# Optimization experiments

Measured on AMD Instinct MI355X. Metric: run time of the kernel, lower is better.

Reference implementation:

```python
import jax, jax.numpy as jnp
import numpy as np

C = 128
NUM_HEADS = 8
KEY_DIM = C // NUM_HEADS  # 16
BN_EPS = 1e-5


def setup_inputs() -> dict:
    key = jax.random.key(0)
    ks = jax.random.split(key, 6)
    B, H, W = 8, 32, 32
    stddev = KEY_DIM ** (-0.5)
    return {
        "x": jax.random.normal(ks[0], (B, C, H, W), dtype=jnp.float32),
        "gamma": jnp.ones((C,), dtype=jnp.float32),
        "beta": jnp.zeros((C,), dtype=jnp.float32),
        "wq": jax.random.normal(ks[1], (C, C), dtype=jnp.float32) * 0.05,
        "wk": jax.random.normal(ks[2], (C, C), dtype=jnp.float32) * 0.05,
        "wv": jax.random.normal(ks[3], (C, C), dtype=jnp.float32) * 0.05,
        "pos_emb_h": jax.random.uniform(ks[4], (2 * H - 1,), dtype=jnp.float32) * stddev,
        "pos_emb_w": jax.random.uniform(ks[5], (2 * W - 1,), dtype=jnp.float32) * stddev,
    }


def _rel_bias(pos_emb, L):
    # torch: pos_emb.unfold(0, L, 1).flip(-1) -> emb[i, k] = pos_emb[i + (L-1) - k]
    idx = jnp.arange(L)[:, None] + (L - 1) - jnp.arange(L)[None, :]
    return pos_emb[idx]  # [L, L]


def reference(x, gamma, beta, wq, wk, wv, pos_emb_h, pos_emb_w):
    B, _, H, W = x.shape
    N = H * W
    qk_scale = 1.0 / np.sqrt(np.float32(KEY_DIM))

    # BatchNorm2d (training-mode batch stats, biased variance) + exact GELU
    mean = jnp.mean(x, axis=(0, 2, 3), keepdims=True)
    var = jnp.var(x, axis=(0, 2, 3), keepdims=True)
    out = (x - mean) * jax.lax.rsqrt(var + BN_EPS)
    out = out * gamma[None, :, None, None] + beta[None, :, None, None]
    out = jax.nn.gelu(out, approximate=False)

    # 1x1 convs == per-pixel linear maps, then split heads and flatten spatial
    def proj(w):
        y = jnp.einsum('oc,bchw->bohw', w, out)
        return y.reshape(B, NUM_HEADS, KEY_DIM, N)  # [B, h, d, N]

    q = proj(wq) * qk_scale
    k = proj(wk)
    v = proj(wv)

    scores = jnp.einsum('bhdq,bhdk->bhqk', q, k)  # [B, h, N, N]

    h_emb = _rel_bias(pos_emb_h, H)  # [H, H]
    w_emb = _rel_bias(pos_emb_w, W)  # [W, W]
    emb = (h_emb[:, None, :, None] + w_emb[None, :, None, :]).reshape(N, N)
    scores = scores + emb[None, None, :, :]

    attn = jax.nn.softmax(scores, axis=-1)
    o = jnp.einsum('bhqk,bhdk->bhdq', attn, v)  # [B, h, d, N]
    o = o.reshape(B, C, H, W)
    return x + o
```

## Files before the change

kernel.cpp:

```cpp
#include <hip/hip_runtime.h>
#include <hip/hip_bf16.h>
#include <math.h>

typedef short bf4 __attribute__((ext_vector_type(4)));
typedef float f32x4 __attribute__((ext_vector_type(4)));

constexpr int CC  = 128;
constexpr int NH  = 8;
constexpr int KD  = 16;
constexpr int BB  = 8;
constexpr int NN  = 1024;
constexpr int BHW = BB * NN;
constexpr float LOG2E = 1.44269504088896340736f;
constexpr float MBOUND = 32.0f;

static __device__ __forceinline__ short f2bf(float x) {
    __hip_bfloat16 b = __float2bfloat16(x);
    short s;
    __builtin_memcpy(&s, &b, 2);
    return s;
}
static __device__ __forceinline__ unsigned fbits(float x) {
    unsigned u;
    __builtin_memcpy(&u, &x, 4);
    return u;
}
static __device__ __forceinline__ float fexp2(float x) {
#if __has_builtin(__builtin_amdgcn_exp2f)
    return __builtin_amdgcn_exp2f(x);
#else
    return exp2f(x);
#endif
}

static __device__ __forceinline__ f32x4 mfma16(bf4 a, bf4 b, f32x4 c) {
#if __has_builtin(__builtin_amdgcn_mfma_f32_16x16x16bf16_1k)
    return __builtin_amdgcn_mfma_f32_16x16x16bf16_1k(a, b, c, 0, 0, 0);
#else
    f32x4 d;
    asm volatile("v_mfma_f32_16x16x16_bf16 %0, %1, %2, %3"
                 : "=&v"(d) : "v"(a), "v"(b), "v"(c));
    return d;
#endif
}

__global__ __launch_bounds__(256) void k_prep(const float* __restrict__ x,
                                              const float* __restrict__ wq,
                                              const float* __restrict__ wk,
                                              const float* __restrict__ wv,
                                              float* __restrict__ ps,
                                              short* __restrict__ wf) {
    int t = threadIdx.x;
    int blk = blockIdx.x;
    if (blk < 1024) {
        int c = blk >> 3, b = blk & 7;
        float4 v = ((const float4*)(x + ((size_t)b * CC + c) * NN))[t];
        float s1 = v.x + v.y + v.z + v.w;
        float s2 = v.x * v.x + v.y * v.y + v.z * v.z + v.w * v.w;
        #pragma unroll
        for (int off = 32; off >= 1; off >>= 1) {
            s1 += __shfl_xor(s1, off);
            s2 += __shfl_xor(s2, off);
        }
        __shared__ float r1[4], r2[4];
        int wid = t >> 6, lane = t & 63;
        if (lane == 0) { r1[wid] = s1; r2[wid] = s2; }
        __syncthreads();
        if (t == 0) {
            ps[(c * 8 + b) * 2 + 0] = r1[0] + r1[1] + r1[2] + r1[3];
            ps[(c * 8 + b) * 2 + 1] = r2[0] + r2[1] + r2[2] + r2[3];
        }
    } else {
        int s = (blk - 1024) * 256 + t;
        int ln = s & 63, ct = (s >> 6) & 7, mt = (s >> 9) & 7, p = s >> 12;
        int hl = ln >> 4, li = ln & 15;
        const float* w = (p == 0) ? wq : (p == 1) ? wk : wv;
        float4 v = *(const float4*)(w + (size_t)(mt * 16 + li) * CC + ct * 16 + 4 * hl);
        float sc = (p == 0) ? 0.25f * LOG2E : 1.0f;
        bf4 r;
        r[0] = f2bf(v.x * sc); r[1] = f2bf(v.y * sc);
        r[2] = f2bf(v.z * sc); r[3] = f2bf(v.w * sc);
        *(bf4*)&wf[(size_t)s * 4] = r;
    }
}

__global__ __launch_bounds__(512) void k_proj(const float* __restrict__ x,
                                              const float* __restrict__ ps,
                                              const float* __restrict__ gamma,
                                              const float* __restrict__ beta,
                                              const short* __restrict__ wf,
                                              short* __restrict__ qf,
                                              short* __restrict__ kf,
                                              short* __restrict__ vf) {
    __shared__ float xS[128][20];
    __shared__ float ssS[256];
    __shared__ short afS[8][256];
    int it = blockIdx.x, b = blockIdx.y;
    int t = threadIdx.x;
    if (t < 128) {
        int c = t;
        const float4* pp = (const float4*)(ps + c * 16);
        float4 a0 = pp[0], a1 = pp[1], a2 = pp[2], a3 = pp[3];
        float s1 = a0.x + a0.z + a1.x + a1.z + a2.x + a2.z + a3.x + a3.z;
        float s2 = a0.y + a0.w + a1.y + a1.w + a2.y + a2.w + a3.y + a3.w;
        float mean = s1 / (float)BHW;
        float var  = s2 / (float)BHW - mean * mean;
        float rstd = rsqrtf(var + 1e-5f);
        float sc = rstd * gamma[c];
        ssS[c]       = sc;
        ssS[128 + c] = beta[c] - mean * sc;
    }
    const float* xb = x + (size_t)b * CC * NN + it * 16;
    {
        int r = t >> 2, cf = t & 3;
        float4 v = *(const float4*)(xb + (size_t)r * NN + cf * 4);
        *(float4*)&xS[r][cf * 4] = v;
    }
    __syncthreads();
    {
        int ct = t >> 6, ln = t & 63;
        int hl_ = ln >> 4, li_ = ln & 15;
        int c0 = ct * 16 + 4 * hl_;
        bf4 r;
        #pragma unroll
        for (int jj = 0; jj < 4; ++jj) {
            int c = c0 + jj;
            float v = xS[c][li_] * ssS[c] + ssS[128 + c];
            v = 0.5f * v * (1.0f + erff(v * 0.70710678f));
            r[jj] = f2bf(v);
        }
        *(bf4*)&afS[ct][ln * 4] = r;
    }
    __syncthreads();

    int wid = t >> 6, lane = t & 63;
    int hl = lane >> 4, li = lane & 15;
    f32x4 acc[3];
    #pragma unroll
    for (int e = 0; e < 3; ++e) acc[e] = (f32x4)0.f;
    #pragma unroll
    for (int ct = 0; ct < 8; ++ct) {
        bf4 af = *(const bf4*)&afS[ct][lane * 4];
        #pragma unroll
        for (int e = 0; e < 3; ++e) {
            int mtp = wid + 8 * e;
            bf4 wfr = *(const bf4*)(wf + ((size_t)(mtp * 8 + ct) * 64 + lane) * 4);
            acc[e] = mfma16(wfr, af, acc[e]);
        }
    }
    int bq = b * 8;
    #pragma unroll
    for (int e = 0; e < 2; ++e) {
        short* dst = (e == 0) ? qf : kf;
        bf4 r;
        #pragma unroll
        for (int jr = 0; jr < 4; ++jr) r[jr] = f2bf(acc[e][jr]);
        *(bf4*)&dst[(((size_t)(bq + wid) * 64 + it) * 64 + lane) * 4] = r;
    }
    {
        float* vScrW = &xS[0][0] + wid * 272;
        #pragma unroll
        for (int r = 0; r < 4; ++r)
            vScrW[(4 * hl + r) * 17 + li] = acc[2][r];
        bf4 r;
        #pragma unroll
        for (int jj = 0; jj < 4; ++jj)
            r[jj] = f2bf(vScrW[li * 17 + 4 * hl + jj]);
        *(bf4*)&vf[(((size_t)(bq + wid) * 64 + it) * 64 + lane) * 4] = r;
    }
}

__global__ __launch_bounds__(512) void k_attn(const short* __restrict__ qf,
                                              const short* __restrict__ kf,
                                              const short* __restrict__ vf,
                                              const float* __restrict__ x,
                                              const float* __restrict__ peh,
                                              const float* __restrict__ pew,
                                              float* __restrict__ out) {
    __shared__ short ldsK[16384];
    __shared__ short ldsV[16384];
    __shared__ float phS[64], pwS[64];
    int t = threadIdx.x;
    int bh = blockIdx.x;
    const short* qfh = qf + (size_t)bh * 16384;
    const short* kfh = kf + (size_t)bh * 16384;
    const short* vfh = vf + (size_t)bh * 16384;

    #pragma unroll
    for (int k = 0; k < 4; ++k)
        ((int4*)ldsK)[t + 512 * k] = ((const int4*)kfh)[t + 512 * k];
    #pragma unroll
    for (int k = 0; k < 4; ++k)
        ((int4*)ldsV)[t + 512 * k] = ((const int4*)vfh)[t + 512 * k];
    if (t < 64) {
        phS[t] = (t < 63) ? peh[t] * LOG2E : -1e30f;
        pwS[t] = (t < 63) ? pew[t] * LOG2E : -1e30f;
    }
    __syncthreads();

    int wid = t >> 6, lane = t & 63;
    int li = lane & 15, hl = lane >> 4;
    int it = blockIdx.y * 8 + wid;

    bf4 qfr = *(const bf4*)(qfh + ((size_t)it * 64 + lane) * 4);

    int wi = ((it & 1) << 4) | li;
    float pwm[2][4];
    #pragma unroll
    for (int jp = 0; jp < 2; ++jp)
        #pragma unroll
        for (int r = 0; r < 4; ++r)
            pwm[jp][r] = pwS[wi + 31 - ((jp << 4) + 4 * hl + r)] - MBOUND;

    int hq = it >> 1;
    const float* phBase = &phS[hq];
    const short* kBase = &ldsK[lane * 4];
    const short* vBase = &ldsV[lane * 4];

    f32x4 oaccA = (f32x4)0.f, oaccB = (f32x4)0.f;
    f32x4 lacc0 = (f32x4)0.f, lacc1 = (f32x4)0.f;
    short oneb = (short)0x3F80;
    bf4 ones = {oneb, oneb, oneb, oneb};

    auto qk = [&](int ch, f32x4* s) {
        float ph0 = phBase[31 - 2 * ch];
        float ph1 = phBase[30 - 2 * ch];
        #pragma unroll
        for (int jt = 0; jt < 4; ++jt) {
            bf4 kb = *(const bf4*)(kBase + (ch * 4 + jt) * 256);
            float ph = (jt < 2) ? ph0 : ph1;
            f32x4 c;
            #pragma unroll
            for (int r = 0; r < 4; ++r) c[r] = pwm[jt & 1][r] + ph;
            s[jt] = mfma16(kb, qfr, c);
        }
    };

    f32x4 s_cur[4];
    qk(0, s_cur);
    #pragma unroll
    for (int ch = 0; ch < 16; ++ch) {
        f32x4 s_nxt[4];
        if (ch < 15) qk(ch + 1, s_nxt);
        bf4 vb[4];
        #pragma unroll
        for (int jt = 0; jt < 4; ++jt)
            vb[jt] = *(const bf4*)(vBase + (ch * 4 + jt) * 256);
        #pragma unroll
        for (int jt = 0; jt < 4; ++jt)
            #pragma unroll
            for (int r = 0; r < 4; ++r)
                s_cur[jt][r] = fexp2(s_cur[jt][r]);
        bf4 pf[4];
        #pragma unroll
        for (int jt = 0; jt < 4; ++jt) {
            unsigned lo = __builtin_amdgcn_perm(fbits(s_cur[jt][1]), fbits(s_cur[jt][0]), 0x07060302u);
            unsigned hi = __builtin_amdgcn_perm(fbits(s_cur[jt][3]), fbits(s_cur[jt][2]), 0x07060302u);
            unsigned pk[2] = {lo, hi};
            __builtin_memcpy(&pf[jt], pk, 8);
        }
        oaccA = mfma16(vb[0], pf[0], oaccA);
        oaccB = mfma16(vb[2], pf[2], oaccB);
        lacc0 = mfma16(ones,  pf[0], lacc0);
        lacc1 = mfma16(ones,  pf[2], lacc1);
        oaccA = mfma16(vb[1], pf[1], oaccA);
        oaccB = mfma16(vb[3], pf[3], oaccB);
        lacc0 = mfma16(ones,  pf[1], lacc0);
        lacc1 = mfma16(ones,  pf[3], lacc1);
        #pragma unroll
        for (int jt = 0; jt < 4; ++jt) s_cur[jt] = s_nxt[jt];
    }

    float rl = 1.0f / (lacc0[0] + lacc1[0]);

    int b = bh >> 3, h = bh & 7;
    size_t base = (size_t)b * (CC * NN) + (size_t)h * KD * NN;
    int i = it * 16 + li;
    #pragma unroll
    for (int r = 0; r < 4; ++r) {
        int d = 4 * hl + r;
        size_t g = base + (size_t)d * NN + i;
        out[g] = x[g] + (oaccA[r] + oaccB[r]) * rl;
    }
}

extern "C" void kernel_launch(void* const* d_in, const int* in_sizes, int n_in,
                              void* d_out, int out_size, void* d_ws, size_t ws_size,
                              hipStream_t stream) {
    const float* x     = (const float*)d_in[0];
    const float* gamma = (const float*)d_in[1];
    const float* beta  = (const float*)d_in[2];
    const float* wq    = (const float*)d_in[3];
    const float* wk    = (const float*)d_in[4];
    const float* wv    = (const float*)d_in[5];
    const float* peh   = (const float*)d_in[6];
    const float* pew   = (const float*)d_in[7];
    float* out = (float*)d_out;
    float* ws  = (float*)d_ws;

    float* ps = ws;
    short* wf = (short*)(ws + 2048);
    short* qf = wf + 49152;
    short* kf = qf + (1 << 20);
    short* vf = kf + (1 << 20);

    k_prep<<<1072, 256, 0, stream>>>(x, wq, wk, wv, ps, wf);
    k_proj<<<dim3(64, 8), 512, 0, stream>>>(x, ps, gamma, beta, wf, qf, kf, vf);
    k_attn<<<dim3(64, 8), 512, 0, stream>>>(qf, kf, vf, x, peh, pew, out);
}
```

Measured before the change: 32.72 us.

## Stage K/V into LDS progressively and overlap staging with attention compute

The attention kernel now loads all K/V tiles into registers up front and writes them to LDS in four phases. Only the first quarter is made visible before compute begins, and each later quarter is stored while the current chunks are processed, with a barrier between phases. This hides the global-to-LDS staging latency behind the MFMA work. It also adds s_setprio around the PV MFMAs and a launch_bounds occupancy hint, at the cost of more registers held across the loop and extra barriers.

```diff
diff --git a/kernel.cpp b/kernel.cpp
--- a/kernel.cpp
+++ b/kernel.cpp
@@ -170,13 +170,13 @@
     }
 }
 
-__global__ __launch_bounds__(512) void k_attn(const short* __restrict__ qf,
-                                              const short* __restrict__ kf,
-                                              const short* __restrict__ vf,
-                                              const float* __restrict__ x,
-                                              const float* __restrict__ peh,
-                                              const float* __restrict__ pew,
-                                              float* __restrict__ out) {
+__global__ __launch_bounds__(512, 4) void k_attn(const short* __restrict__ qf,
+                                                 const short* __restrict__ kf,
+                                                 const short* __restrict__ vf,
+                                                 const float* __restrict__ x,
+                                                 const float* __restrict__ peh,
+                                                 const float* __restrict__ pew,
+                                                 float* __restrict__ out) {
     __shared__ short ldsK[16384];
     __shared__ short ldsV[16384];
     __shared__ float phS[64], pwS[64];
@@ -186,23 +186,25 @@
     const short* kfh = kf + (size_t)bh * 16384;
     const short* vfh = vf + (size_t)bh * 16384;
 
-    #pragma unroll
-    for (int k = 0; k < 4; ++k)
-        ((int4*)ldsK)[t + 512 * k] = ((const int4*)kfh)[t + 512 * k];
-    #pragma unroll
-    for (int k = 0; k < 4; ++k)
-        ((int4*)ldsV)[t + 512 * k] = ((const int4*)vfh)[t + 512 * k];
+    int4 kreg[4], vreg[4];
+    #pragma unroll
+    for (int k = 0; k < 4; ++k) kreg[k] = ((const int4*)kfh)[t + 512 * k];
+    #pragma unroll
+    for (int k = 0; k < 4; ++k) vreg[k] = ((const int4*)vfh)[t + 512 * k];
     if (t < 64) {
         phS[t] = (t < 63) ? peh[t] * LOG2E : -1e30f;
         pwS[t] = (t < 63) ? pew[t] * LOG2E : -1e30f;
     }
-    __syncthreads();
 
     int wid = t >> 6, lane = t & 63;
     int li = lane & 15, hl = lane >> 4;
     int it = blockIdx.y * 8 + wid;
-
     bf4 qfr = *(const bf4*)(qfh + ((size_t)it * 64 + lane) * 4);
+
+    ((int4*)ldsK)[t] = kreg[0];
+    ((int4*)ldsV)[t] = vreg[0];
+    asm volatile("s_waitcnt lgkmcnt(0)" ::: "memory");
+    __builtin_amdgcn_s_barrier();
 
     int wi = ((it & 1) << 4) | li;
     float pwm[2][4];
@@ -235,13 +237,7 @@
             s[jt] = mfma16(kb, qfr, c);
         }
     };
-
-    f32x4 s_cur[4];
-    qk(0, s_cur);
-    #pragma unroll
-    for (int ch = 0; ch < 16; ++ch) {
-        f32x4 s_nxt[4];
-        if (ch < 15) qk(ch + 1, s_nxt);
+    auto body = [&](f32x4* s_cur, int ch) {
         bf4 vb[4];
         #pragma unroll
         for (int jt = 0; jt < 4; ++jt)
@@ -259,6 +255,7 @@
             unsigned pk[2] = {lo, hi};
             __builtin_memcpy(&pf[jt], pk, 8);
         }
+        __builtin_amdgcn_s_setprio(1);
         oaccA = mfma16(vb[0], pf[0], oaccA);
         oaccB = mfma16(vb[2], pf[2], oaccB);
         lacc0 = mfma16(ones,  pf[0], lacc0);
@@ -267,8 +264,33 @@
         oaccB = mfma16(vb[3], pf[3], oaccB);
         lacc0 = mfma16(ones,  pf[1], lacc0);
         lacc1 = mfma16(ones,  pf[3], lacc1);
-        #pragma unroll
-        for (int jt = 0; jt < 4; ++jt) s_cur[jt] = s_nxt[jt];
+        __builtin_amdgcn_s_setprio(0);
+    };
+
+    f32x4 s_cur[4];
+    qk(0, s_cur);
+    #pragma unroll
+    for (int p = 0; p < 4; ++p) {
+        if (p < 3) {
+            ((int4*)ldsK)[t + 512 * (p + 1)] = kreg[p + 1];
+            ((int4*)ldsV)[t + 512 * (p + 1)] = vreg[p + 1];
+        }
+        #pragma unroll
+        for (int c = 0; c < 4; ++c) {
+            int ch = 4 * p + c;
+            f32x4 s_nxt[4];
+            if (c < 3) qk(ch + 1, s_nxt);
+            body(s_cur, ch);
+            if (c < 3) {
+                #pragma unroll
+                for (int jt = 0; jt < 4; ++jt) s_cur[jt] = s_nxt[jt];
+            }
+        }
+        if (p < 3) {
+            asm volatile("s_waitcnt lgkmcnt(0)" ::: "memory");
+            __builtin_amdgcn_s_barrier();
+            qk(4 * (p + 1), s_cur);
+        }
     }
 
     float rl = 1.0f / (lacc0[0] + lacc1[0]);
```

Result: no change. 32.78 us (+0.2%).

## Process two query tiles per wave in attention, reuse K/V fragments

Applied to the files above, without the earlier changes.

Each wave in the attention kernel now handles two 16-query tiles, so each K and V LDS fragment load feeds two MFMAs and the grid halves in y. The software-pipelined QK prefetch is removed in favour of interleaving the two independent tiles, and s_setprio is raised around the PV MFMA block. The projection kernel writes Q/K/V with nontemporal stores, and launch bounds now request 2 blocks per CU. Fewer workgroups and higher register pressure could reduce parallelism across the GPU.

```diff
diff --git a/kernel.cpp b/kernel.cpp
--- a/kernel.cpp
+++ b/kernel.cpp
@@ -155,7 +155,8 @@
         bf4 r;
         #pragma unroll
         for (int jr = 0; jr < 4; ++jr) r[jr] = f2bf(acc[e][jr]);
-        *(bf4*)&dst[(((size_t)(bq + wid) * 64 + it) * 64 + lane) * 4] = r;
+        __builtin_nontemporal_store(r,
+            (bf4*)&dst[(((size_t)(bq + wid) * 64 + it) * 64 + lane) * 4]);
     }
     {
         float* vScrW = &xS[0][0] + wid * 272;
@@ -166,17 +167,18 @@
         #pragma unroll
         for (int jj = 0; jj < 4; ++jj)
             r[jj] = f2bf(vScrW[li * 17 + 4 * hl + jj]);
-        *(bf4*)&vf[(((size_t)(bq + wid) * 64 + it) * 64 + lane) * 4] = r;
-    }
-}
-
-__global__ __launch_bounds__(512) void k_attn(const short* __restrict__ qf,
-                                              const short* __restrict__ kf,
-                                              const short* __restrict__ vf,
-                                              const float* __restrict__ x,
-                                              const float* __restrict__ peh,
-                                              const float* __restrict__ pew,
-                                              float* __restrict__ out) {
+        __builtin_nontemporal_store(r,
+            (bf4*)&vf[(((size_t)(bq + wid) * 64 + it) * 64 + lane) * 4]);
+    }
+}
+
+__global__ __launch_bounds__(512, 2) void k_attn(const short* __restrict__ qf,
+                                                 const short* __restrict__ kf,
+                                                 const short* __restrict__ vf,
+                                                 const float* __restrict__ x,
+                                                 const float* __restrict__ peh,
+                                                 const float* __restrict__ pew,
+                                                 float* __restrict__ out) {
     __shared__ short ldsK[16384];
     __shared__ short ldsV[16384];
     __shared__ float phS[64], pwS[64];
@@ -200,87 +202,104 @@
 
     int wid = t >> 6, lane = t & 63;
     int li = lane & 15, hl = lane >> 4;
-    int it = blockIdx.y * 8 + wid;
-
-    bf4 qfr = *(const bf4*)(qfh + ((size_t)it * 64 + lane) * 4);
-
-    int wi = ((it & 1) << 4) | li;
-    float pwm[2][4];
+    int it0 = (blockIdx.y * 8 + wid) * 2;
+
+    bf4 qfrA = *(const bf4*)(qfh + ((size_t)it0 * 64 + lane) * 4);
+    bf4 qfrB = *(const bf4*)(qfh + ((size_t)(it0 + 1) * 64 + lane) * 4);
+
+    float pwmA[2][4], pwmB[2][4];
     #pragma unroll
     for (int jp = 0; jp < 2; ++jp)
         #pragma unroll
-        for (int r = 0; r < 4; ++r)
-            pwm[jp][r] = pwS[wi + 31 - ((jp << 4) + 4 * hl + r)] - MBOUND;
-
-    int hq = it >> 1;
+        for (int r = 0; r < 4; ++r) {
+            int wj = (jp << 4) + 4 * hl + r;
+            pwmA[jp][r] = pwS[li + 31 - wj] - MBOUND;
+            pwmB[jp][r] = pwS[16 + li + 31 - wj] - MBOUND;
+        }
+
+    int hq = it0 >> 1;
     const float* phBase = &phS[hq];
     const short* kBase = &ldsK[lane * 4];
     const short* vBase = &ldsV[lane * 4];
 
-    f32x4 oaccA = (f32x4)0.f, oaccB = (f32x4)0.f;
-    f32x4 lacc0 = (f32x4)0.f, lacc1 = (f32x4)0.f;
+    f32x4 oA0 = (f32x4)0.f, oA1 = (f32x4)0.f, lA0 = (f32x4)0.f, lA1 = (f32x4)0.f;
+    f32x4 oB0 = (f32x4)0.f, oB1 = (f32x4)0.f, lB0 = (f32x4)0.f, lB1 = (f32x4)0.f;
     short oneb = (short)0x3F80;
     bf4 ones = {oneb, oneb, oneb, oneb};
 
-    auto qk = [&](int ch, f32x4* s) {
+    #pragma unroll
+    for (int ch = 0; ch < 16; ++ch) {
         float ph0 = phBase[31 - 2 * ch];
         float ph1 = phBase[30 - 2 * ch];
+        bf4 kb[4], vb[4];
         #pragma unroll
         for (int jt = 0; jt < 4; ++jt) {
-            bf4 kb = *(const bf4*)(kBase + (ch * 4 + jt) * 256);
+            kb[jt] = *(const bf4*)(kBase + (ch * 4 + jt) * 256);
+            vb[jt] = *(const bf4*)(vBase + (ch * 4 + jt) * 256);
+        }
+        f32x4 sA[4], sB[4];
+        #pragma unroll
+        for (int jt = 0; jt < 4; ++jt) {
             float ph = (jt < 2) ? ph0 : ph1;
-            f32x4 c;
+            f32x4 cA, cB;
             #pragma unroll
-            for (int r = 0; r < 4; ++r) c[r] = pwm[jt & 1][r] + ph;
-            s[jt] = mfma16(kb, qfr, c);
-        }
-    };
-
-    f32x4 s_cur[4];
-    qk(0, s_cur);
-    #pragma unroll
-    for (int ch = 0; ch < 16; ++ch) {
-        f32x4 s_nxt[4];
-        if (ch < 15) qk(ch + 1, s_nxt);
-        bf4 vb[4];
-        #pragma unroll
-        for (int jt = 0; jt < 4; ++jt)
-            vb[jt] = *(const bf4*)(vBase + (ch * 4 + jt) * 256);
+            for (int r = 0; r < 4; ++r) {
+                cA[r] = pwmA[jt & 1][r] + ph;
+                cB[r] = pwmB[jt & 1][r] + ph;
+            }
+            sA[jt] = mfma16(kb[jt], qfrA, cA);
+            sB[jt] = mfma16(kb[jt], qfrB, cB);
+        }
         #pragma unroll
         for (int jt = 0; jt < 4; ++jt)
             #pragma unroll
-            for (int r = 0; r < 4; ++r)
-                s_cur[jt][r] = fexp2(s_cur[jt][r]);
-        bf4 pf[4];
+            for (int r = 0; r < 4; ++r) {
+                sA[jt][r] = fexp2(sA[jt][r]);
+                sB[jt][r] = fexp2(sB[jt][r]);
+            }
+        bf4 pfA[4], pfB[4];
         #pragma unroll
         for (int jt = 0; jt < 4; ++jt) {
-            unsigned lo = __builtin_amdgcn_perm(fbits(s_cur[jt][1]), fbits(s_cur[jt][0]), 0x07060302u);
-            unsigned hi = __builtin_amdgcn_perm(fbits(s_cur[jt][3]), fbits(s_cur[jt][2]), 0x07060302u);
-            unsigned pk[2] = {lo, hi};
-            __builtin_memcpy(&pf[jt], pk, 8);
-        }
-        oaccA = mfma16(vb[0], pf[0], oaccA);
-        oaccB = mfma16(vb[2], pf[2], oaccB);
-        lacc0 = mfma16(ones,  pf[0], lacc0);
-        lacc1 = mfma16(ones,  pf[2], lacc1);
-        oaccA = mfma16(vb[1], pf[1], oaccA);
-        oaccB = mfma16(vb[3], pf[3], oaccB);
-        lacc0 = mfma16(ones,  pf[1], lacc0);
-        lacc1 = mfma16(ones,  pf[3], lacc1);
-        #pragma unroll
-        for (int jt = 0; jt < 4; ++jt) s_cur[jt] = s_nxt[jt];
-    }
-
-    float rl = 1.0f / (lacc0[0] + lacc1[0]);
+            unsigned loA = __builtin_amdgcn_perm(fbits(sA[jt][1]), fbits(sA[jt][0]), 0x07060302u);
+            unsigned hiA = __builtin_amdgcn_perm(fbits(sA[jt][3]), fbits(sA[jt][2]), 0x07060302u);
+            unsigned pkA[2] = {loA, hiA};
+            __builtin_memcpy(&pfA[jt], pkA, 8);
+            unsigned loB = __builtin_amdgcn_perm(fbits(sB[jt][1]), fbits(sB[jt][0]), 0x07060302u);
+            unsigned hiB = __builtin_amdgcn_perm(fbits(sB[jt][3]), fbits(sB[jt][2]), 0x07060302u);
+            unsigned pkB[2] = {loB, hiB};
+            __builtin_memcpy(&pfB[jt], pkB, 8);
+        }
+        __builtin_amdgcn_s_setprio(1);
+        oA0 = mfma16(vb[0], pfA[0], oA0);
+        oB0 = mfma16(vb[0], pfB[0], oB0);
+        oA1 = mfma16(vb[2], pfA[2], oA1);
+        oB1 = mfma16(vb[2], pfB[2], oB1);
+        lA0 = mfma16(ones,  pfA[0], lA0);
+        lB0 = mfma16(ones,  pfB[0], lB0);
+        lA1 = mfma16(ones,  pfA[2], lA1);
+        lB1 = mfma16(ones,  pfB[2], lB1);
+        oA0 = mfma16(vb[1], pfA[1], oA0);
+        oB0 = mfma16(vb[1], pfB[1], oB0);
+        oA1 = mfma16(vb[3], pfA[3], oA1);
+        oB1 = mfma16(vb[3], pfB[3], oB1);
+        lA0 = mfma16(ones,  pfA[1], lA0);
+        lB0 = mfma16(ones,  pfB[1], lB0);
+        lA1 = mfma16(ones,  pfA[3], lA1);
+        lB1 = mfma16(ones,  pfB[3], lB1);
+        __builtin_amdgcn_s_setprio(0);
+    }
+
+    float rlA = 1.0f / (lA0[0] + lA1[0]);
+    float rlB = 1.0f / (lB0[0] + lB1[0]);
 
     int b = bh >> 3, h = bh & 7;
     size_t base = (size_t)b * (CC * NN) + (size_t)h * KD * NN;
-    int i = it * 16 + li;
+    int iA = it0 * 16 + li;
     #pragma unroll
     for (int r = 0; r < 4; ++r) {
-        int d = 4 * hl + r;
-        size_t g = base + (size_t)d * NN + i;
-        out[g] = x[g] + (oaccA[r] + oaccB[r]) * rl;
+        size_t g = base + (size_t)(4 * hl + r) * NN + iA;
+        out[g]      = x[g]      + (oA0[r] + oA1[r]) * rlA;
+        out[g + 16] = x[g + 16] + (oB0[r] + oB1[r]) * rlB;
     }
 }
 
@@ -306,5 +325,5 @@
 
     k_prep<<<1072, 256, 0, stream>>>(x, wq, wk, wv, ps, wf);
     k_proj<<<dim3(64, 8), 512, 0, stream>>>(x, ps, gamma, beta, wf, qf, kf, vf);
-    k_attn<<<dim3(64, 8), 512, 0, stream>>>(qf, kf, vf, x, peh, pew, out);
-}
+    k_attn<<<dim3(64, 4), 512, 0, stream>>>(qf, kf, vf, x, peh, pew, out);
+}
```

Measured after the change: 32.57 us. No clear change (-0.5%).

## Software-pipeline attention loop two chunks deep with MFMA priority and nontemporal stores

Applied to the files above, without the earlier changes.

Restructures the attention inner loop into a two-stage ping-pong pipeline, so the QK MFMAs for chunk ch+2 and ch+3 are issued while the exp/pack and PV MFMAs of earlier chunks run. It raises wave priority around the PV MFMA block with s_setprio. It also adds a min-blocks hint to launch_bounds and switches the projection kernel's q/k/v stores to nontemporal. This is meant to hide exp latency behind matrix-core work. In exchange it holds more registers live, and the occupancy hint may force register spills.

```diff
diff --git a/kernel.cpp b/kernel.cpp
--- a/kernel.cpp
+++ b/kernel.cpp
@@ -155,7 +155,8 @@
         bf4 r;
         #pragma unroll
         for (int jr = 0; jr < 4; ++jr) r[jr] = f2bf(acc[e][jr]);
-        *(bf4*)&dst[(((size_t)(bq + wid) * 64 + it) * 64 + lane) * 4] = r;
+        __builtin_nontemporal_store(r,
+            (bf4*)&dst[(((size_t)(bq + wid) * 64 + it) * 64 + lane) * 4]);
     }
     {
         float* vScrW = &xS[0][0] + wid * 272;
@@ -166,17 +167,18 @@
         #pragma unroll
         for (int jj = 0; jj < 4; ++jj)
             r[jj] = f2bf(vScrW[li * 17 + 4 * hl + jj]);
-        *(bf4*)&vf[(((size_t)(bq + wid) * 64 + it) * 64 + lane) * 4] = r;
-    }
-}
-
-__global__ __launch_bounds__(512) void k_attn(const short* __restrict__ qf,
-                                              const short* __restrict__ kf,
-                                              const short* __restrict__ vf,
-                                              const float* __restrict__ x,
-                                              const float* __restrict__ peh,
-                                              const float* __restrict__ pew,
-                                              float* __restrict__ out) {
+        __builtin_nontemporal_store(r,
+            (bf4*)&vf[(((size_t)(bq + wid) * 64 + it) * 64 + lane) * 4]);
+    }
+}
+
+__global__ __launch_bounds__(512, 4) void k_attn(const short* __restrict__ qf,
+                                                 const short* __restrict__ kf,
+                                                 const short* __restrict__ vf,
+                                                 const float* __restrict__ x,
+                                                 const float* __restrict__ peh,
+                                                 const float* __restrict__ pew,
+                                                 float* __restrict__ out) {
     __shared__ short ldsK[16384];
     __shared__ short ldsV[16384];
     __shared__ float phS[64], pwS[64];
@@ -235,14 +237,7 @@
             s[jt] = mfma16(kb, qfr, c);
         }
     };
-
-    f32x4 s_cur[4];
-    qk(0, s_cur);
-    #pragma unroll
-    for (int ch = 0; ch < 16; ++ch) {
-        f32x4 s_nxt[4];
-        if (ch < 15) qk(ch + 1, s_nxt);
-        bf4 vb[4];
+    auto stage = [&](f32x4* s, bf4* pf, bf4* vb, int ch) {
         #pragma unroll
         for (int jt = 0; jt < 4; ++jt)
             vb[jt] = *(const bf4*)(vBase + (ch * 4 + jt) * 256);
@@ -250,15 +245,17 @@
         for (int jt = 0; jt < 4; ++jt)
             #pragma unroll
             for (int r = 0; r < 4; ++r)
-                s_cur[jt][r] = fexp2(s_cur[jt][r]);
-        bf4 pf[4];
+                s[jt][r] = fexp2(s[jt][r]);
         #pragma unroll
         for (int jt = 0; jt < 4; ++jt) {
-            unsigned lo = __builtin_amdgcn_perm(fbits(s_cur[jt][1]), fbits(s_cur[jt][0]), 0x07060302u);
-            unsigned hi = __builtin_amdgcn_perm(fbits(s_cur[jt][3]), fbits(s_cur[jt][2]), 0x07060302u);
+            unsigned lo = __builtin_amdgcn_perm(fbits(s[jt][1]), fbits(s[jt][0]), 0x07060302u);
+            unsigned hi = __builtin_amdgcn_perm(fbits(s[jt][3]), fbits(s[jt][2]), 0x07060302u);
             unsigned pk[2] = {lo, hi};
             __builtin_memcpy(&pf[jt], pk, 8);
         }
+    };
+    auto pv = [&](bf4* vb, bf4* pf) {
+        __builtin_amdgcn_s_setprio(1);
         oaccA = mfma16(vb[0], pf[0], oaccA);
         oaccB = mfma16(vb[2], pf[2], oaccB);
         lacc0 = mfma16(ones,  pf[0], lacc0);
@@ -267,8 +264,23 @@
         oaccB = mfma16(vb[3], pf[3], oaccB);
         lacc0 = mfma16(ones,  pf[1], lacc0);
         lacc1 = mfma16(ones,  pf[3], lacc1);
-        #pragma unroll
-        for (int jt = 0; jt < 4; ++jt) s_cur[jt] = s_nxt[jt];
+        __builtin_amdgcn_s_setprio(0);
+    };
+
+    f32x4 sA[4], sB[4];
+    bf4 pfA[4], pfB[4], vbA[4], vbB[4];
+    qk(0, sA);
+    stage(sA, pfA, vbA, 0);
+    qk(1, sB);
+    #pragma unroll
+    for (int h2 = 0; h2 < 8; ++h2) {
+        int ch = 2 * h2;
+        if (ch + 2 < 16) qk(ch + 2, sA);
+        pv(vbA, pfA);
+        if (ch + 1 < 16) stage(sB, pfB, vbB, ch + 1);
+        if (ch + 3 < 16) qk(ch + 3, sB);
+        pv(vbB, pfB);
+        if (ch + 2 < 16) stage(sA, pfA, vbA, ch + 2);
     }
 
     float rl = 1.0f / (lacc0[0] + lacc1[0]);
```

New measurement: 35.47 us. 1.08x slower.
